# Kernel tuning notes

Hardware: AMD Instinct MI355X
Metric: run time of the kernel (lower is better)

Reference implementation:

```python
import jax, jax.numpy as jnp
import numpy as np

D_MODEL = 1024
NUM_HEADS = 16
D_K = D_MODEL // NUM_HEADS
B, S = 2, 2048


def setup_inputs() -> dict:
    key = jax.random.key(0)
    ks = jax.random.split(key, 6)
    scale = 1.0 / np.sqrt(D_MODEL)
    x = jax.random.normal(ks[0], (B, S, D_MODEL), dtype=jnp.float32)
    # causal mask: 1 where masked (future positions), per masked_fill(mask == 1, -inf)
    mask = jnp.triu(jnp.ones((S, S), dtype=jnp.int32), k=1)
    Wq = jax.random.normal(ks[1], (D_MODEL, D_MODEL), dtype=jnp.float32) * scale
    Wk = jax.random.normal(ks[2], (D_MODEL, D_MODEL), dtype=jnp.float32) * scale
    Wv = jax.random.normal(ks[3], (D_MODEL, D_MODEL), dtype=jnp.float32) * scale
    Wo = jax.random.normal(ks[4], (D_MODEL, D_MODEL), dtype=jnp.float32) * scale
    zeros = jnp.zeros((D_MODEL,), dtype=jnp.float32)
    return {"x": x, "mask": mask, "Wq": Wq, "bq": zeros, "Wk": Wk, "bk": zeros,
            "Wv": Wv, "bv": zeros, "Wo": Wo, "bo": zeros}


def reference(x, mask, Wq, bq, Wk, bk, Wv, bv, Wo, bo):
    b, s, d = x.shape
    # linear projections (torch nn.Linear: x @ W^T + b; here W stored as [in, out])
    Q = x @ Wq + bq
    K = x @ Wk + bk
    V = x @ Wv + bv
    # split heads -> (b, h, s, d_k)
    def split(t):
        return t.reshape(b, s, NUM_HEADS, D_K).transpose(0, 2, 1, 3)
    Q, K, V = split(Q), split(K), split(V)
    scale = 1.0 / jnp.sqrt(jnp.float32(D_K))
    scores = jnp.einsum("bhqd,bhkd->bhqk", Q, K) * scale  # (b,h,s,s)
    scores = jnp.where(mask[None, None, :, :] == 1, -jnp.inf, scores)
    attn = jax.nn.softmax(scores, axis=-1)
    out = jnp.einsum("bhqk,bhkd->bhqd", attn, V)
    out = out.transpose(0, 2, 1, 3).reshape(b, s, d)  # concat heads
    return out @ Wo + bo
```

## Files before the change

### kernel.cpp

```cpp
#include <hip/hip_runtime.h>
#include <hip/hip_bf16.h>
#include <cstdint>
#include <cmath>

#define DM 1024
#define NH 16
#define DK 64
#define NB 2
#define SS 2048
#define MM (NB*SS)

typedef unsigned short u16;
typedef uint32_t u32;
typedef __attribute__((ext_vector_type(4))) float f32x4;
typedef __attribute__((ext_vector_type(8))) short s16x8;
typedef __attribute__((ext_vector_type(2))) uint32_t u32x2;

__device__ __forceinline__ u16 f2bf(float f) {
    __hip_bfloat16 h = __float2bfloat16(f);
    return __builtin_bit_cast(u16, h);
}
__device__ __forceinline__ float bf2f(u16 u) {
    u32 x = (u32)u << 16;
    return __builtin_bit_cast(float, x);
}

__device__ __forceinline__ u32 cvtpk(float a, float b) {
    u32 r;
    asm("v_cvt_pk_bf16_f32 %0, %1, %2" : "=v"(r) : "v"(a), "v"(b));
    return r;
}

__device__ __forceinline__ void gload_lds16(void* lds, const void* g) {
    __builtin_amdgcn_global_load_lds(
        (const __attribute__((address_space(1))) uint32_t*)g,
        (__attribute__((address_space(3))) uint32_t*)lds, 16, 0, 0);
}

__device__ __forceinline__ int swz(int row, int cb) {
    return row * 128 + ((((cb) >> 4) ^ (row & 7)) << 4) + ((cb) & 15);
}

#define FENCE_BAR  do { __builtin_amdgcn_sched_barrier(0); \
                        __builtin_amdgcn_s_barrier();      \
                        __builtin_amdgcn_sched_barrier(0); } while (0)

__global__ void mha_prep(const float* __restrict__ x, u16* __restrict__ xb,
                         const float* __restrict__ W0, const float* __restrict__ W1,
                         const float* __restrict__ W2, const float* __restrict__ W3,
                         u16* __restrict__ WtBase) {
    const int bid = blockIdx.x, tid = threadIdx.x;
    if (bid < 4096) {
        int i = (bid * 256 + tid) * 4;
        float4 v = *reinterpret_cast<const float4*>(x + i);
        ushort4 o;
        o.x = f2bf(v.x); o.y = f2bf(v.y); o.z = f2bf(v.z); o.w = f2bf(v.w);
        *reinterpret_cast<ushort4*>(xb + i) = o;
        return;
    }
    __shared__ float t[32][33];
    const int b2 = bid - 4096;
    const int mat = b2 >> 10, rem = b2 & 1023;
    const int cx = rem & 31, cy = rem >> 5;
    const float* W = (mat == 0) ? W0 : (mat == 1) ? W1 : (mat == 2) ? W2 : W3;
    u16* Wt = WtBase + (size_t)mat * DM * DM;
    const int c0 = cx * 32, r0 = cy * 32;
    const int tx = tid & 31, ty = tid >> 5;
#pragma unroll
    for (int i = ty; i < 32; i += 8)
        t[i][tx] = W[(size_t)(r0 + i) * DM + c0 + tx];
    __syncthreads();
#pragma unroll
    for (int i = ty; i < 32; i += 8)
        Wt[(size_t)(c0 + i) * DM + r0 + tx] = f2bf(t[tx][i]);
}

__device__ __forceinline__ void gemm_loop(const u16* __restrict__ A, const u16* __restrict__ Bt,
                                          int m0, int n0,
                                          u16 (*As)[64], u16 (*Bs)[64], f32x4 acc[4][4]) {
    const int tid = threadIdx.x;
    const int wave = tid >> 6, lane = tid & 63;
    const int lr = lane & 15, kg = lane >> 4;
    const int wr = wave >> 1, wc = wave & 1;

    for (int k0 = 0; k0 < DM; k0 += 64) {
        __syncthreads();
#pragma unroll
        for (int i = 0; i < 4; ++i) {
            const int o   = ((wave * 4 + i) * 64 + lane) * 16;
            const int row = o >> 7;
            const int kb  = o & 127;
            gload_lds16((char*)As + o, A  + (size_t)(m0 + row) * DM + k0 + (kb >> 1));
            gload_lds16((char*)Bs + o, Bt + (size_t)(n0 + row) * DM + k0 + (kb >> 1));
        }
        __syncthreads();
#pragma unroll
        for (int kk = 0; kk < 64; kk += 32) {
            s16x8 a[4], b[4];
#pragma unroll
            for (int m = 0; m < 4; ++m)
                a[m] = *reinterpret_cast<const s16x8*>(&As[wr * 64 + m * 16 + lr][kk + kg * 8]);
#pragma unroll
            for (int n = 0; n < 4; ++n)
                b[n] = *reinterpret_cast<const s16x8*>(&Bs[wc * 64 + n * 16 + lr][kk + kg * 8]);
#pragma unroll
            for (int m = 0; m < 4; ++m)
#pragma unroll
                for (int n = 0; n < 4; ++n)
                    acc[m][n] = __builtin_amdgcn_mfma_f32_16x16x32_bf16(a[m], b[n], acc[m][n], 0, 0, 0);
        }
    }
}

__global__ __launch_bounds__(256, 2) void mha_gemm_qkv(const u16* __restrict__ xb, const u16* __restrict__ Wt,
                                                       const float* __restrict__ bq, const float* __restrict__ bk,
                                                       const float* __restrict__ bv, u16* __restrict__ qkv) {
    __shared__ __align__(16) char smem[32768];
    u16 (*As)[64] = reinterpret_cast<u16(*)[64]>(smem);
    u16 (*Bs)[64] = reinterpret_cast<u16(*)[64]>(smem + 16384);

    const int bid = blockIdx.x;
    const int j = bid & 7, r = bid >> 3;
    const int bx = j * 4 + (r & 3);
    const int by = (r >> 2) & 7;
    const int z  = r >> 5;
    const int m0 = bx * 128, n0 = by * 128;

    const float* bias = (z == 0) ? bq : (z == 1) ? bk : bv;
    const float scale = (z == 0) ? 0.125f * 1.44269504088896f : 1.0f;
    u16* Cout = qkv + (size_t)z * MM * DM;

    f32x4 acc[4][4] = {};
    gemm_loop(xb, Wt + (size_t)z * DM * DM, m0, n0, As, Bs, acc);

    const int tid = threadIdx.x;
    const int wave = tid >> 6, lane = tid & 63;
    const int lr = lane & 15, kg = lane >> 4;
    const int wr = wave >> 1, wc = wave & 1;

    __syncthreads();
#pragma unroll
    for (int m = 0; m < 4; ++m)
#pragma unroll
        for (int n = 0; n < 4; ++n) {
            const int col = wc * 64 + n * 16 + lr;
            const float bv2 = bias[n0 + col];
#pragma unroll
            for (int j2 = 0; j2 < 4; ++j2) {
                const int row = wr * 64 + m * 16 + kg * 4 + j2;
                const float v = (acc[m][n][j2] + bv2) * scale;
                int imgoff;
                if (z == 0) {
                    imgoff = row * 256 + (col >> 6) * 128 + (col & 63) * 2;
                } else if (z == 1) {
                    imgoff = ((row >> 6) * 2 + (col >> 6)) * 8192 + swz(row & 63, (col & 63) * 2);
                } else {
                    imgoff = ((row >> 6) * 2 + (col >> 6)) * 8192
                           + swz(col & 63, ((row & 63) >> 1) * 4 + (row & 1) * 2);
                }
                *reinterpret_cast<u16*>(smem + imgoff) = f2bf(v);
            }
        }
    __syncthreads();
    const int bb = m0 >> 11, s0 = m0 & (SS - 1);
    const int kt0 = s0 >> 6, h0 = n0 >> 6;
#pragma unroll
    for (int it = 0; it < 8; ++it) {
        const int c = it * 256 + tid;
        const s16x8 v = *reinterpret_cast<const s16x8*>(smem + c * 16);
        u16* dst;
        if (z == 0) {
            const int srow = c >> 4, inrow = c & 15;
            const int hl = inrow >> 3, d0 = (inrow & 7) * 8;
            dst = Cout + (((size_t)(bb * NH + h0 + hl) * SS + (s0 + srow)) * DK) + d0;
        } else {
            const int quad = c >> 9, off = (c & 511) * 8;
            const int ktl = quad >> 1, hl = quad & 1;
            dst = Cout + ((size_t)(bb * NH + h0 + hl) * 32 + kt0 + ktl) * 4096 + off;
        }
        *reinterpret_cast<s16x8*>(dst) = v;
    }
}

__device__ __forceinline__ void gemm_loop_db(const u16* __restrict__ A, const u16* __restrict__ Bt,
                                             int m0, int n0, char* smem , f32x4 acc[4][4]) {
    const int tid = threadIdx.x;
    const int wave = tid >> 6, lane = tid & 63;
    const int lr = lane & 15, kg = lane >> 4;
    const int wr = wave >> 1, wc = wave & 1;

    auto STAGE = [&](int buf, int k0) {
        char* As = smem + buf * 32768;
        char* Bs = As + 16384;
#pragma unroll
        for (int i = 0; i < 4; ++i) {
            const int o   = ((wave * 4 + i) * 64 + lane) * 16;
            const int row = o >> 7;
            const int kb  = o & 127;
            gload_lds16(As + o, A  + (size_t)(m0 + row) * DM + k0 + (kb >> 1));
            gload_lds16(Bs + o, Bt + (size_t)(n0 + row) * DM + k0 + (kb >> 1));
        }
    };

    STAGE(0, 0);
    for (int t = 0; t < 16; ++t) {
        if (t + 1 < 16) {
            STAGE((t + 1) & 1, (t + 1) * 64);
            asm volatile("s_waitcnt vmcnt(8)" ::: "memory");
        } else {
            asm volatile("s_waitcnt vmcnt(0)" ::: "memory");
        }
        FENCE_BAR;
        const u16 (*As)[64] = reinterpret_cast<const u16(*)[64]>(smem + (t & 1) * 32768);
        const u16 (*Bs)[64] = reinterpret_cast<const u16(*)[64]>(smem + (t & 1) * 32768 + 16384);
#pragma unroll
        for (int kk = 0; kk < 64; kk += 32) {
            s16x8 a[4], b[4];
#pragma unroll
            for (int m = 0; m < 4; ++m)
                a[m] = *reinterpret_cast<const s16x8*>(&As[wr * 64 + m * 16 + lr][kk + kg * 8]);
#pragma unroll
            for (int n = 0; n < 4; ++n)
                b[n] = *reinterpret_cast<const s16x8*>(&Bs[wc * 64 + n * 16 + lr][kk + kg * 8]);
#pragma unroll
            for (int m = 0; m < 4; ++m)
#pragma unroll
                for (int n = 0; n < 4; ++n)
                    acc[m][n] = __builtin_amdgcn_mfma_f32_16x16x32_bf16(a[m], b[n], acc[m][n], 0, 0, 0);
        }
        FENCE_BAR;
    }
}

__global__ __launch_bounds__(256, 2) void mha_gemm_out(const u16* __restrict__ AO, const u16* __restrict__ WoT,
                                                       const float* __restrict__ bo, float* __restrict__ out) {
    __shared__ __align__(16) char smem[65536];
    const int m0 = blockIdx.x * 128, n0 = blockIdx.y * 128;

    f32x4 acc[4][4] = {};
    gemm_loop_db(AO, WoT, m0, n0, smem, acc);

    const int tid = threadIdx.x;
    const int wave = tid >> 6, lane = tid & 63;
    const int lr = lane & 15, kg = lane >> 4;
    const int wr = wave >> 1, wc = wave & 1;
#pragma unroll
    for (int m = 0; m < 4; ++m)
#pragma unroll
        for (int n = 0; n < 4; ++n) {
            const int col = n0 + wc * 64 + n * 16 + lr;
            const float bv = bo[col];
#pragma unroll
            for (int j2 = 0; j2 < 4; ++j2) {
                const int row = m0 + wr * 64 + m * 16 + kg * 4 + j2;
                out[(size_t)row * DM + col] = acc[m][n][j2] + bv;
            }
        }
}

__device__ const unsigned char JQT[48] = {
    15,31,30,31, 14,29,30,28,29, 13,27,28,26,27, 12,25,26,24,25,
    11,23,24,22,23, 10,21,22,20,21, 9,19,20,18,19, 8,17,18,16,17,
    7,16, 6,5,4,3,2,1,0};
__device__ const unsigned char JKS[48] = {
    0,0,15,16, 0,0,0,14,15, 0,0,0,13,14, 0,0,0,12,13,
    0,0,0,11,12, 0,0,0,10,11, 0,0,0,9,10, 0,0,0,8,9,
    0,0, 0,0,0,0,0,0,0};
__device__ const unsigned char JKL[48] = {
    16,16,16,16, 15,15,15,15,15, 14,14,14,14,14, 13,13,13,13,13,
    12,12,12,12,12, 11,11,11,11,11, 10,10,10,10,10, 9,9,9,9,9,
    8,8, 7,6,5,4,3,2,1};
__device__ const unsigned char JSL[48] = {
    255,30,29,31, 255,26,28,25,27, 255,22,24,21,23, 255,18,20,17,19,
    255,14,16,13,15, 255,10,12,9,11, 255,6,8,5,7, 255,2,4,1,3,
    255,0, 255,255,255,255,255,255,255};

__global__ __launch_bounds__(256, 4) void mha_attn(const u16* __restrict__ Qb, const u16* __restrict__ Kswz,
                                                   const u16* __restrict__ Vtswz, u16* __restrict__ AO,
                                                   u16* __restrict__ Opart, float* __restrict__ lpart) {
    __shared__ __align__(16) char lds[40960];

    const int bid = blockIdx.x;
    const int bh  = bid & 31;
    const int job = bid >> 5;
    const int qt   = JQT[job];
    const int kst  = JKS[job];
    const int klen = JKL[job];
    const int slot = JSL[job];
    const int qb = qt * 64;

    const int tid = threadIdx.x, w = tid >> 6, lane = tid & 63;
    const int lr = lane & 15, kg = lane >> 4;

    const u16* Qh = Qb + (size_t)bh * SS * DK;
    const char* Ktiles = (const char*)(Kswz  + (size_t)bh * 32 * 4096);
    const char* Vtiles = (const char*)(Vtswz + (size_t)bh * 32 * 4096);
    const int bb = bh >> 4, hh = bh & (NH - 1);
    char* psb = lds + 32768 + w * 2048;
    const int o = tid * 16;

    const int qrow = qb + w * 16 + lr;
    const s16x8 qf0 = *reinterpret_cast<const s16x8*>(Qh + (size_t)qrow * DK + kg * 8);
    const s16x8 qf1 = *reinterpret_cast<const s16x8*>(Qh + (size_t)qrow * DK + 32 + kg * 8);
    f32x4 accO[4] = {};
    float lp = 0.f;

    const int kend = kst + klen;
    {
        const char* Kt = Ktiles + kst * 8192;
        const char* Vt = Vtiles + kst * 8192;
        gload_lds16(lds + o,                 Kt + o);
        gload_lds16(lds + o + 4096,          Kt + o + 4096);
        gload_lds16(lds + 16384 + o,         Vt + o);
        gload_lds16(lds + 16384 + o + 4096,  Vt + o + 4096);
    }

    for (int t = kst; t < kend; ++t) {
        const int buf = (t - kst) & 1;
        asm volatile("s_waitcnt vmcnt(0)" ::: "memory");
        __syncthreads();
        if (t + 1 < kend) {
            const char* Kt = Ktiles + (t + 1) * 8192;
            const char* Vt = Vtiles + (t + 1) * 8192;
            char* kb2 = lds + (buf ^ 1) * 8192;
            char* vb2 = lds + 16384 + (buf ^ 1) * 8192;
            gload_lds16(kb2 + o,        Kt + o);
            gload_lds16(kb2 + o + 4096, Kt + o + 4096);
            gload_lds16(vb2 + o,        Vt + o);
            gload_lds16(vb2 + o + 4096, Vt + o + 4096);
        }
        const char* ksb = lds + buf * 8192;
        const char* vtb = lds + 16384 + buf * 8192;

        f32x4 sc[4];
#pragma unroll
        for (int f = 0; f < 4; ++f) {
            s16x8 kf0 = *reinterpret_cast<const s16x8*>(ksb + swz(f * 16 + lr, kg * 16));
            s16x8 kf1 = *reinterpret_cast<const s16x8*>(ksb + swz(f * 16 + lr, 64 + kg * 16));
            f32x4 s = {};
            s = __builtin_amdgcn_mfma_f32_16x16x32_bf16(kf0, qf0, s, 0, 0, 0);
            s = __builtin_amdgcn_mfma_f32_16x16x32_bf16(kf1, qf1, s, 0, 0, 0);
            sc[f] = s;
        }
#pragma unroll
        for (int f = 0; f < 4; ++f)
#pragma unroll
            for (int j = 0; j < 4; ++j)
                sc[f][j] = __builtin_amdgcn_exp2f(sc[f][j]);
        if (t == qt) {
            const int qloc = w * 16 + lr;
#pragma unroll
            for (int f = 0; f < 4; ++f) {
                const int kc = f * 16 + kg * 4;
#pragma unroll
                for (int j = 0; j < 4; ++j)
                    if (kc + j > qloc) sc[f][j] = 0.f;
            }
        }
        float fs0 = 0.f, fs1 = 0.f;
#pragma unroll
        for (int f = 0; f < 4; ++f) {
            u32x2 pp;
            pp[0] = cvtpk(sc[f][0], sc[f][1]);
            pp[1] = cvtpk(sc[f][2], sc[f][3]);
            *reinterpret_cast<u32x2*>(psb + swz(lr, f * 32 + kg * 8)) = pp;
            const float s01 = sc[f][0] + sc[f][1], s23 = sc[f][2] + sc[f][3];
            if (f & 1) fs1 += s01 + s23; else fs0 += s01 + s23;
        }
        lp += fs0 + fs1;

        const s16x8 pf0 = *reinterpret_cast<const s16x8*>(psb + swz(lr, kg * 16));
        const s16x8 pf1 = *reinterpret_cast<const s16x8*>(psb + swz(lr, 64 + kg * 16));
#pragma unroll
        for (int db = 0; db < 4; ++db) {
            s16x8 vf0 = *reinterpret_cast<const s16x8*>(vtb + swz(db * 16 + lr, kg * 16));
            s16x8 vf1 = *reinterpret_cast<const s16x8*>(vtb + swz(db * 16 + lr, 64 + kg * 16));
            accO[db] = __builtin_amdgcn_mfma_f32_16x16x32_bf16(pf0, vf0, accO[db], 0, 0, 0);
            accO[db] = __builtin_amdgcn_mfma_f32_16x16x32_bf16(pf1, vf1, accO[db], 0, 0, 0);
        }
    }

    lp += __shfl_xor(lp, 16, 64);
    lp += __shfl_xor(lp, 32, 64);

    if (slot == 255) {
        float inv[4];
#pragma unroll
        for (int j = 0; j < 4; ++j)
            inv[j] = 1.0f / __shfl(lp, kg * 4 + j, 64);
#pragma unroll
        for (int db = 0; db < 4; ++db) {
            const int d = db * 16 + lr;
#pragma unroll
            for (int j = 0; j < 4; ++j) {
                const int s = qb + w * 16 + kg * 4 + j;
                AO[((size_t)(bb * SS + s)) * DM + hh * DK + d] = f2bf(accO[db][j] * inv[j]);
            }
        }
    } else {
        const int idx = bh * 32 + slot;
        u16* Od = Opart + (size_t)idx * 4096;
#pragma unroll
        for (int db = 0; db < 4; ++db) {
            const int d = db * 16 + lr;
#pragma unroll
            for (int j = 0; j < 4; ++j)
                Od[(w * 16 + kg * 4 + j) * 64 + d] = f2bf(accO[db][j]);
        }
        if (lane < 16)
            lpart[idx * 64 + w * 16 + lane] = lp;
    }
}

__global__ __launch_bounds__(256) void mha_combine(const u16* __restrict__ Opart,
                                                   const float* __restrict__ lpart,
                                                   u16* __restrict__ AO) {
    const int blk = blockIdx.x;
    const int bh = blk & 31, q = blk >> 5;
    const int qt = 16 + q;
    const int t = threadIdx.x;
    const int row = t >> 2, c0 = (t & 3) * 16;
    const int idx0 = bh * 32 + q * 2;
    const u16* O0 = Opart + (size_t)idx0 * 4096 + row * 64 + c0;
    const u16* O1 = O0 + 4096;
    const float l = lpart[idx0 * 64 + row] + lpart[(idx0 + 1) * 64 + row];
    const float inv = 1.0f / l;
    const int bb = bh >> 4, hh = bh & (NH - 1);
    const int s = qt * 64 + row;
    u16* dst = AO + ((size_t)(bb * SS + s)) * DM + hh * DK + c0;
#pragma unroll
    for (int h = 0; h < 2; ++h) {
        s16x8 a = *reinterpret_cast<const s16x8*>(O0 + h * 8);
        s16x8 b = *reinterpret_cast<const s16x8*>(O1 + h * 8);
        u16* ap = (u16*)&a; u16* bp = (u16*)&b;
        u16 ov[8];
#pragma unroll
    for (int i = 0; i < 8; ++i)
            ov[i] = f2bf((bf2f(ap[i]) + bf2f(bp[i])) * inv);
        *reinterpret_cast<ushort4*>(dst + h * 8) = *reinterpret_cast<ushort4*>(&ov[0]);
        *reinterpret_cast<ushort4*>(dst + h * 8 + 4) = *reinterpret_cast<ushort4*>(&ov[4]);
    }
}

extern "C" void kernel_launch(void* const* d_in, const int* in_sizes, int n_in,
                              void* d_out, int out_size, void* d_ws, size_t ws_size,
                              hipStream_t stream) {
    const float* x  = (const float*)d_in[0];
    const float* Wq = (const float*)d_in[2];
    const float* bq = (const float*)d_in[3];
    const float* Wk = (const float*)d_in[4];
    const float* bk = (const float*)d_in[5];
    const float* Wv = (const float*)d_in[6];
    const float* bv = (const float*)d_in[7];
    const float* Wo = (const float*)d_in[8];
    const float* bo = (const float*)d_in[9];
    float* out = (float*)d_out;

    char* ws = (char*)d_ws;
    u16* xb  = (u16*)(ws);
    u16* Wt  = (u16*)(ws + ((size_t)8  << 20));
    u16* qkv = (u16*)(ws + ((size_t)16 << 20));
    u16* AO  = (u16*)(ws + ((size_t)40 << 20));
    u16*   Opart = (u16*)(ws);
    float* lpart = (float*)(ws + ((size_t)8 << 20));

    mha_prep<<<dim3(8192), dim3(256), 0, stream>>>(x, xb, Wq, Wk, Wv, Wo, Wt);
    mha_gemm_qkv<<<dim3(768), dim3(256), 0, stream>>>(xb, Wt, bq, bk, bv, qkv);
    mha_attn<<<dim3(1536), dim3(256), 0, stream>>>(qkv, qkv + (size_t)4194304, qkv + (size_t)8388608,
                                                   AO, Opart, lpart);
    mha_combine<<<dim3(512), dim3(256), 0, stream>>>(Opart, lpart, AO);
    mha_gemm_out<<<dim3(32, 8), dim3(256), 0, stream>>>(AO, Wt + (size_t)3 * DM * DM, bo, out);
}
```

Measured before the change: 103.5 us.

## Double attention query tile to 128 rows with 512-thread blocks

The attention kernel now processes 128 query rows per block using 8 waves of 512 threads. Each K/V tile loaded into LDS is therefore shared by twice as many query rows, which halves the K/V global traffic per query. The work-split tables, causal masking, partial-output indexing and the combine kernel are all rewritten for the larger tile and the smaller grid. In exchange there are fewer blocks to balance the triangular causal workload, larger LDS use, and a mask check that now runs on more than one tile.

New measurement: 102.7 us. Within noise of the previous version (-0.8%).

```diff
diff --git a/kernel.cpp b/kernel.cpp
--- a/kernel.cpp
+++ b/kernel.cpp
@@ -258,27 +258,19 @@
         }
 }
 
-__device__ const unsigned char JQT[48] = {
-    15,31,30,31, 14,29,30,28,29, 13,27,28,26,27, 12,25,26,24,25,
-    11,23,24,22,23, 10,21,22,20,21, 9,19,20,18,19, 8,17,18,16,17,
-    7,16, 6,5,4,3,2,1,0};
-__device__ const unsigned char JKS[48] = {
-    0,0,15,16, 0,0,0,14,15, 0,0,0,13,14, 0,0,0,12,13,
-    0,0,0,11,12, 0,0,0,10,11, 0,0,0,9,10, 0,0,0,8,9,
-    0,0, 0,0,0,0,0,0,0};
-__device__ const unsigned char JKL[48] = {
-    16,16,16,16, 15,15,15,15,15, 14,14,14,14,14, 13,13,13,13,13,
-    12,12,12,12,12, 11,11,11,11,11, 10,10,10,10,10, 9,9,9,9,9,
-    8,8, 7,6,5,4,3,2,1};
-__device__ const unsigned char JSL[48] = {
-    255,30,29,31, 255,26,28,25,27, 255,22,24,21,23, 255,18,20,17,19,
-    255,14,16,13,15, 255,10,12,9,11, 255,6,8,5,7, 255,2,4,1,3,
-    255,0, 255,255,255,255,255,255,255};
-
-__global__ __launch_bounds__(256, 4) void mha_attn(const u16* __restrict__ Qb, const u16* __restrict__ Kswz,
+__device__ const unsigned char JQT[24] = {
+    7,15,15, 14,14, 6,13,13, 12,12, 5,11,11, 10,10, 4,9,9, 8,8, 3,2,1,0};
+__device__ const unsigned char JKS[24] = {
+    0,0,16, 0,15, 0,0,14, 0,13, 0,0,12, 0,11, 0,0,10, 0,9, 0,0,0,0};
+__device__ const unsigned char JKL[24] = {
+    16,16,16, 15,15, 14,14,14, 13,13, 12,12,12, 11,11, 10,10,10, 9,9, 8,6,4,2};
+__device__ const unsigned char JSL[24] = {
+    255,14,15, 12,13, 255,10,11, 8,9, 255,6,7, 4,5, 255,2,3, 0,1, 255,255,255,255};
+
+__global__ __launch_bounds__(512, 4) void mha_attn(const u16* __restrict__ Qb, const u16* __restrict__ Kswz,
                                                    const u16* __restrict__ Vtswz, u16* __restrict__ AO,
                                                    u16* __restrict__ Opart, float* __restrict__ lpart) {
-    __shared__ __align__(16) char lds[40960];
+    __shared__ __align__(16) char lds[49152];
 
     const int bid = blockIdx.x;
     const int bh  = bid & 31;
@@ -287,7 +279,7 @@
     const int kst  = JKS[job];
     const int klen = JKL[job];
     const int slot = JSL[job];
-    const int qb = qt * 64;
+    const int qb = qt * 128;
 
     const int tid = threadIdx.x, w = tid >> 6, lane = tid & 63;
     const int lr = lane & 15, kg = lane >> 4;
@@ -306,31 +298,20 @@
     float lp = 0.f;
 
     const int kend = kst + klen;
-    {
-        const char* Kt = Ktiles + kst * 8192;
-        const char* Vt = Vtiles + kst * 8192;
-        gload_lds16(lds + o,                 Kt + o);
-        gload_lds16(lds + o + 4096,          Kt + o + 4096);
-        gload_lds16(lds + 16384 + o,         Vt + o);
-        gload_lds16(lds + 16384 + o + 4096,  Vt + o + 4096);
-    }
+    gload_lds16(lds + o,         Ktiles + kst * 8192 + o);
+    gload_lds16(lds + 16384 + o, Vtiles + kst * 8192 + o);
 
     for (int t = kst; t < kend; ++t) {
         const int buf = (t - kst) & 1;
         asm volatile("s_waitcnt vmcnt(0)" ::: "memory");
         __syncthreads();
         if (t + 1 < kend) {
-            const char* Kt = Ktiles + (t + 1) * 8192;
-            const char* Vt = Vtiles + (t + 1) * 8192;
-            char* kb2 = lds + (buf ^ 1) * 8192;
-            char* vb2 = lds + 16384 + (buf ^ 1) * 8192;
-            gload_lds16(kb2 + o,        Kt + o);
-            gload_lds16(kb2 + o + 4096, Kt + o + 4096);
-            gload_lds16(vb2 + o,        Vt + o);
-            gload_lds16(vb2 + o + 4096, Vt + o + 4096);
+            gload_lds16(lds + (buf ^ 1) * 8192 + o,         Ktiles + (t + 1) * 8192 + o);
+            gload_lds16(lds + 16384 + (buf ^ 1) * 8192 + o, Vtiles + (t + 1) * 8192 + o);
         }
         const char* ksb = lds + buf * 8192;
         const char* vtb = lds + 16384 + buf * 8192;
+        const int kb = t * 64;
 
         f32x4 sc[4];
 #pragma unroll
@@ -347,14 +328,14 @@
 #pragma unroll
             for (int j = 0; j < 4; ++j)
                 sc[f][j] = __builtin_amdgcn_exp2f(sc[f][j]);
-        if (t == qt) {
-            const int qloc = w * 16 + lr;
+        if (kb + 63 > qb + w * 16) {
+            const int qg = qb + w * 16 + lr;
 #pragma unroll
             for (int f = 0; f < 4; ++f) {
-                const int kc = f * 16 + kg * 4;
+                const int kc = kb + f * 16 + kg * 4;
 #pragma unroll
                 for (int j = 0; j < 4; ++j)
-                    if (kc + j > qloc) sc[f][j] = 0.f;
+                    if (kc + j > qg) sc[f][j] = 0.f;
             }
         }
         float fs0 = 0.f, fs1 = 0.f;
@@ -398,8 +379,8 @@
             }
         }
     } else {
-        const int idx = bh * 32 + slot;
-        u16* Od = Opart + (size_t)idx * 4096;
+        const int idx = bh * 16 + slot;
+        u16* Od = Opart + (size_t)idx * 8192;
 #pragma unroll
         for (int db = 0; db < 4; ++db) {
             const int d = db * 16 + lr;
@@ -408,7 +389,7 @@
                 Od[(w * 16 + kg * 4 + j) * 64 + d] = f2bf(accO[db][j]);
         }
         if (lane < 16)
-            lpart[idx * 64 + w * 16 + lane] = lp;
+            lpart[idx * 128 + w * 16 + lane] = lp;
     }
 }
 
@@ -417,25 +398,25 @@
                                                    u16* __restrict__ AO) {
     const int blk = blockIdx.x;
     const int bh = blk & 31, q = blk >> 5;
-    const int qt = 16 + q;
+    const int qt = 8 + q;
     const int t = threadIdx.x;
-    const int row = t >> 2, c0 = (t & 3) * 16;
-    const int idx0 = bh * 32 + q * 2;
-    const u16* O0 = Opart + (size_t)idx0 * 4096 + row * 64 + c0;
-    const u16* O1 = O0 + 4096;
-    const float l = lpart[idx0 * 64 + row] + lpart[(idx0 + 1) * 64 + row];
+    const int row = t >> 1, c0 = (t & 1) * 32;
+    const int idx0 = bh * 16 + q * 2;
+    const u16* O0 = Opart + (size_t)idx0 * 8192 + row * 64 + c0;
+    const u16* O1 = O0 + 8192;
+    const float l = lpart[idx0 * 128 + row] + lpart[(idx0 + 1) * 128 + row];
     const float inv = 1.0f / l;
     const int bb = bh >> 4, hh = bh & (NH - 1);
-    const int s = qt * 64 + row;
+    const int s = qt * 128 + row;
     u16* dst = AO + ((size_t)(bb * SS + s)) * DM + hh * DK + c0;
 #pragma unroll
-    for (int h = 0; h < 2; ++h) {
+    for (int h = 0; h < 4; ++h) {
         s16x8 a = *reinterpret_cast<const s16x8*>(O0 + h * 8);
         s16x8 b = *reinterpret_cast<const s16x8*>(O1 + h * 8);
         u16* ap = (u16*)&a; u16* bp = (u16*)&b;
         u16 ov[8];
 #pragma unroll
-    for (int i = 0; i < 8; ++i)
+        for (int i = 0; i < 8; ++i)
             ov[i] = f2bf((bf2f(ap[i]) + bf2f(bp[i])) * inv);
         *reinterpret_cast<ushort4*>(dst + h * 8) = *reinterpret_cast<ushort4*>(&ov[0]);
         *reinterpret_cast<ushort4*>(dst + h * 8 + 4) = *reinterpret_cast<ushort4*>(&ov[4]);
@@ -466,8 +447,8 @@
 
     mha_prep<<<dim3(8192), dim3(256), 0, stream>>>(x, xb, Wq, Wk, Wv, Wo, Wt);
     mha_gemm_qkv<<<dim3(768), dim3(256), 0, stream>>>(xb, Wt, bq, bk, bv, qkv);
-    mha_attn<<<dim3(1536), dim3(256), 0, stream>>>(qkv, qkv + (size_t)4194304, qkv + (size_t)8388608,
-                                                   AO, Opart, lpart);
-    mha_combine<<<dim3(512), dim3(256), 0, stream>>>(Opart, lpart, AO);
+    mha_attn<<<dim3(768), dim3(512), 0, stream>>>(qkv, qkv + (size_t)4194304, qkv + (size_t)8388608,
+                                                  AO, Opart, lpart);
+    mha_combine<<<dim3(256), dim3(256), 0, stream>>>(Opart, lpart, AO);
     mha_gemm_out<<<dim3(32, 8), dim3(256), 0, stream>>>(AO, Wt + (size_t)3 * DM * DM, bo, out);
 }
```
